# Kernel tuning notes

Measured on AMD Instinct MI355X. Metric: run time of the kernel, lower is better.

The kernel has to match this reference:

```python
import jax, jax.numpy as jnp
import numpy as np

B, S, D = 1, 4096, 2048
M = 4                  # compression rate
NC = S // M            # compressed slots
TOPK = 512
NH, C = 16, 64         # query heads, head dim
DC = 512               # query compression dim
NG, DG = 4, 512        # output projection groups, intermediate dim
CI, NHI = 64, 4        # indexer head dim, indexer heads
ROPE = 32              # partial rope dims (last ROPE of C)
EPS = 1e-6
NEG = -1e30


def _ln(x, w, b):
    mu = x.mean(-1, keepdims=True)
    var = ((x - mu) ** 2).mean(-1, keepdims=True)
    return (x - mu) * jax.lax.rsqrt(var + EPS) * w + b


def _rope(q, pos):
    # partial RoPE on the last ROPE dims of q [B,S,NH,C]; keys are NOT rotated (faithful)
    x_part, x_rope = q[..., :C - ROPE], q[..., C - ROPE:]
    x0, x1 = x_rope[..., 0::2], x_rope[..., 1::2]
    inv = 1.0 / (10000.0 ** (jnp.arange(0, ROPE, 2, dtype=jnp.float32) / ROPE))
    ang = pos[:, None].astype(jnp.float32) * inv[None]           # [S, ROPE/2]
    cos = jnp.cos(ang)[None, :, None, :]
    sin = jnp.sin(ang)[None, :, None, :]
    r = x0 * cos - x1 * sin
    i = x0 * sin + x1 * cos
    rot = jnp.stack([r, i], -1).reshape(x_rope.shape)
    return jnp.concatenate([x_part, rot], -1)


def reference(x, w_kv_a, w_kv_b, w_z_a, w_z_b, b_a, b_b, w_dq, w_iuq, w_w, w_k,
              w_uq, o_down, o_up, kvn_w, kvn_b, qn_w, qn_b, sink_logits):
    pos = jnp.arange(S)
    # ---- token-level compressor: windowed (2m-wide, m-stride) per-channel softmax ----
    c_a = (x @ w_kv_a).reshape(B, NC, M, C)
    c_b = (x @ w_kv_b).reshape(B, NC, M, C)
    z_a = (x @ w_z_a).reshape(B, NC, M, C)
    z_b = (x @ w_z_b).reshape(B, NC, M, C)
    prev_z = jnp.concatenate([jnp.full((B, 1, M, C), NEG, x.dtype), z_b[:, :-1]], 1)
    prev_c = jnp.concatenate([jnp.zeros((B, 1, M, C), x.dtype), c_b[:, :-1]], 1)
    logits = jnp.concatenate([prev_z + b_b, z_a + b_a], 2)        # [B,NC,2M,C]
    wts = jax.nn.softmax(logits, axis=2)
    compressed = (wts * jnp.concatenate([prev_c, c_a], 2)).sum(2)  # [B,NC,C]
    # ---- lightning indexer: relu multi-head scores + causal mask + top-k ----
    c_q = x @ w_dq                                                 # [B,S,DC]
    q_i = (c_q @ w_iuq).reshape(B, S, NHI, CI)
    hw = x @ w_w                                                   # [B,S,NHI]
    k_orig = x.reshape(B, NC, M, D).mean(2)
    k_proj = k_orig @ w_k                                          # [B,NC,CI]
    dot = jnp.einsum('bshc,bkc->bskh', q_i, k_proj)
    iscores = (jax.nn.relu(dot) * hw[:, :, None, :]).sum(-1)       # [B,S,NC]
    imask = jnp.arange(NC)[None, None, :] < pos[None, :, None]     # NC//S + 1 == 1
    iscores = jnp.where(imask, iscores, -jnp.inf)
    _, top_idx = jax.lax.top_k(iscores, TOPK)                      # [B,S,K]
    # ---- sparse attention over gathered compressed KV ----
    q = (c_q @ w_uq).reshape(B, S, NH, C)
    kc = _ln(compressed, kvn_w, kvn_b)
    q = _rope(_ln(q, qn_w, qn_b), pos)
    k_sel = kc[jnp.arange(B)[:, None, None], top_idx]              # [B,S,K,C]
    scores = jnp.einsum('bshc,bskc->bhsk', q, k_sel) / jnp.sqrt(jnp.float32(C))
    cmask = pos[None, None, :, None] < (top_idx[:, None, :, :] * M)
    scores = jnp.where(cmask, scores, -jnp.inf)
    e = jnp.exp(scores)
    denom = e.sum(-1, keepdims=True) + jnp.exp(sink_logits)[None, :, None, None]
    attn = e / denom                                               # sink-augmented softmax
    out = jnp.einsum('bhsk,bskc->bshc', attn, k_sel).reshape(B, S, NH * C)
    g = jnp.einsum('bsgd,gde->bsge', out.reshape(B, S, NG, (NH * C) // NG), o_down)
    return g.reshape(B, S, NG * DG) @ o_up


def setup_inputs() -> dict:
    key = jax.random.key(0)
    ks = jax.random.split(key, 20)
    lin = lambda k, fi, fo: jax.random.normal(k, (fi, fo), jnp.float32) / np.sqrt(fi)
    return {
        'x': jax.random.normal(ks[0], (B, S, D), jnp.float32),
        'w_kv_a': lin(ks[1], D, C), 'w_kv_b': lin(ks[2], D, C),
        'w_z_a': lin(ks[3], D, C), 'w_z_b': lin(ks[4], D, C),
        'b_a': 0.02 * jax.random.normal(ks[5], (M, C), jnp.float32),
        'b_b': 0.02 * jax.random.normal(ks[6], (M, C), jnp.float32),
        'w_dq': lin(ks[7], D, DC),
        'w_iuq': lin(ks[8], DC, CI * NHI),
        'w_w': lin(ks[9], D, NHI),
        'w_k': lin(ks[10], D, CI),
        'w_uq': lin(ks[11], DC, NH * C),
        'o_down': jax.random.normal(ks[12], (NG, (NH * C) // NG, DG), jnp.float32) / np.sqrt((NH * C) // NG),
        'o_up': lin(ks[13], NG * DG, D),
        'kvn_w': 1.0 + 0.02 * jax.random.normal(ks[14], (C,), jnp.float32),
        'kvn_b': 0.02 * jax.random.normal(ks[15], (C,), jnp.float32),
        'qn_w': 1.0 + 0.02 * jax.random.normal(ks[16], (C,), jnp.float32),
        'qn_b': 0.02 * jax.random.normal(ks[17], (C,), jnp.float32),
        'sink_logits': 0.02 * jax.random.normal(ks[18], (NH,), jnp.float32),
    }
```

## Files before the change

kernel.cpp:

```cpp
#include <hip/hip_runtime.h>
#include <math.h>

#define S_   4096
#define D_   2048
#define M_   4
#define NC_  1024
#define TOPK_ 512
#define NH_  16
#define C_   64
#define DC_  512
#define NG_  4
#define DG_  512
#define CI_  64
#define NHI_ 4
#define ROPE_ 32
#define EPS_ 1e-6f

typedef __attribute__((ext_vector_type(8))) short short8;
typedef __attribute__((ext_vector_type(4))) short short4v;
typedef __attribute__((ext_vector_type(4))) float floatx4;

__device__ inline unsigned short f2bf(float f) {
  unsigned u = __float_as_uint(f);
  u += 0x7fff + ((u >> 16) & 1);
  return (unsigned short)(u >> 16);
}
__device__ inline float bf2f(unsigned short h) {
  return __uint_as_float(((unsigned)h) << 16);
}

#define GLD16(src, dst) __builtin_amdgcn_global_load_lds( \
    (const __attribute__((address_space(1))) unsigned int*)(src), \
    (__attribute__((address_space(3))) unsigned int*)(dst), 16, 0, 0)

__global__ __launch_bounds__(256) void gemm_bf16_64(
    const unsigned short* __restrict__ A, const unsigned short* __restrict__ Bt,
    float* __restrict__ Cf, unsigned short* __restrict__ Cb,
    int K, int lda, int ldb, int ldc,
    long long Az, long long Bz, long long Cz) {
  int zz = blockIdx.z;
  A += (size_t)zz * Az;
  Bt += (size_t)zz * Bz;
  if (Cf) Cf += (size_t)zz * Cz;
  if (Cb) Cb += (size_t)zz * Cz;
  __shared__ unsigned short As[2 * 2 * 64 * 32];
  __shared__ unsigned short Bs[2 * 2 * 128 * 32];
  int tid = threadIdx.x;
  int bm = blockIdx.y * 64, bn = blockIdx.x * 128;
  int lane = tid & 63, wid = tid >> 6;
  int wm = (wid & 1) * 32, wn = (wid >> 1) * 64;
  int qd = lane >> 4, m16 = lane & 15;

  floatx4 acc[2][4];
#pragma unroll
  for (int i = 0; i < 2; ++i)
#pragma unroll
    for (int j = 0; j < 4; ++j) acc[i][j] = (floatx4){0.f, 0.f, 0.f, 0.f};

  auto stage = [&](int buf, int kt) {
#pragma unroll
    for (int h = 0; h < 2; ++h) {
      {
        int rr = tid >> 2, ss = tid & 3;
        int gg = ss ^ ((rr >> 1) & 3);
        GLD16(A + (size_t)(bm + rr) * lda + kt + h * 32 + gg * 8,
              &As[(buf * 2 + h) * 2048 + tid * 8]);
      }
#pragma unroll
      for (int i = 0; i < 2; ++i) {
        int idx = tid + 256 * i;
        int rr = idx >> 2, ss = idx & 3;
        int gg = ss ^ ((rr >> 1) & 3);
        GLD16(Bt + (size_t)(bn + rr) * ldb + kt + h * 32 + gg * 8,
              &Bs[(buf * 2 + h) * 4096 + idx * 8]);
      }
    }
  };
  auto compute = [&](int buf) {
#pragma unroll
    for (int h = 0; h < 2; ++h) {
      const unsigned short* Ab = &As[(buf * 2 + h) * 2048];
      const unsigned short* Bb = &Bs[(buf * 2 + h) * 4096];
      short8 af[2], bfr[4];
#pragma unroll
      for (int mi = 0; mi < 2; ++mi) {
        int r = wm + mi * 16 + m16;
        int slot = qd ^ ((r >> 1) & 3);
        af[mi] = *(const short8*)&Ab[r * 32 + slot * 8];
      }
#pragma unroll
      for (int ni = 0; ni < 4; ++ni) {
        int r = wn + ni * 16 + m16;
        int slot = qd ^ ((r >> 1) & 3);
        bfr[ni] = *(const short8*)&Bb[r * 32 + slot * 8];
      }
#pragma unroll
      for (int mi = 0; mi < 2; ++mi)
#pragma unroll
        for (int ni = 0; ni < 4; ++ni)
          acc[mi][ni] = __builtin_amdgcn_mfma_f32_16x16x32_bf16(af[mi], bfr[ni], acc[mi][ni], 0, 0, 0);
    }
  };

  stage(0, 0);
  __syncthreads();
  int cur = 0;
  for (int kt = 64; kt < K; kt += 64) {
    stage(cur ^ 1, kt);
    compute(cur);
    __syncthreads();
    cur ^= 1;
  }
  compute(cur);

#pragma unroll
  for (int mi = 0; mi < 2; ++mi)
#pragma unroll
    for (int ni = 0; ni < 4; ++ni) {
      int col = bn + wn + ni * 16 + m16;
#pragma unroll
      for (int rg = 0; rg < 4; ++rg) {
        int row = bm + wm + mi * 16 + qd * 4 + rg;
        if (Cb)
          Cb[(size_t)row * ldc + col] = f2bf(acc[mi][ni][rg]);
        else
          Cf[(size_t)row * ldc + col] = acc[mi][ni][rg];
      }
    }
}

__global__ __launch_bounds__(256) void gemm_bf16_128(
    const unsigned short* __restrict__ A, const unsigned short* __restrict__ Bt,
    float* __restrict__ Cf, unsigned short* __restrict__ Cb,
    int K, int lda, int ldb, int ldc,
    long long Az, long long Bz, long long Cz) {
  int zz = blockIdx.z;
  A += (size_t)zz * Az;
  Bt += (size_t)zz * Bz;
  if (Cf) Cf += (size_t)zz * Cz;
  if (Cb) Cb += (size_t)zz * Cz;
  __shared__ unsigned short As[2 * 2 * 128 * 32];
  __shared__ unsigned short Bs[2 * 2 * 128 * 32];
  int tid = threadIdx.x;
  int bm = blockIdx.y * 128, bn = blockIdx.x * 128;
  int lane = tid & 63, wid = tid >> 6;
  int wm = (wid & 1) * 64, wn = (wid >> 1) * 64;
  int qd = lane >> 4, m16 = lane & 15;

  floatx4 acc[4][4];
#pragma unroll
  for (int i = 0; i < 4; ++i)
#pragma unroll
    for (int j = 0; j < 4; ++j) acc[i][j] = (floatx4){0.f, 0.f, 0.f, 0.f};

  auto stage = [&](int buf, int kt) {
#pragma unroll
    for (int h = 0; h < 2; ++h) {
#pragma unroll
      for (int i = 0; i < 2; ++i) {
        int idx = tid + 256 * i;
        int rr = idx >> 2, ss = idx & 3;
        int gg = ss ^ ((rr >> 1) & 3);
        GLD16(A + (size_t)(bm + rr) * lda + kt + h * 32 + gg * 8,
              &As[(buf * 2 + h) * 4096 + idx * 8]);
        GLD16(Bt + (size_t)(bn + rr) * ldb + kt + h * 32 + gg * 8,
              &Bs[(buf * 2 + h) * 4096 + idx * 8]);
      }
    }
  };
  auto compute = [&](int buf) {
#pragma unroll
    for (int h = 0; h < 2; ++h) {
      const unsigned short* Ab = &As[(buf * 2 + h) * 4096];
      const unsigned short* Bb = &Bs[(buf * 2 + h) * 4096];
      short8 af[4], bfr[4];
#pragma unroll
      for (int mi = 0; mi < 4; ++mi) {
        int r = wm + mi * 16 + m16;
        int slot = qd ^ ((r >> 1) & 3);
        af[mi] = *(const short8*)&Ab[r * 32 + slot * 8];
      }
#pragma unroll
      for (int ni = 0; ni < 4; ++ni) {
        int r = wn + ni * 16 + m16;
        int slot = qd ^ ((r >> 1) & 3);
        bfr[ni] = *(const short8*)&Bb[r * 32 + slot * 8];
      }
#pragma unroll
      for (int mi = 0; mi < 4; ++mi)
#pragma unroll
        for (int ni = 0; ni < 4; ++ni)
          acc[mi][ni] = __builtin_amdgcn_mfma_f32_16x16x32_bf16(af[mi], bfr[ni], acc[mi][ni], 0, 0, 0);
    }
  };

  stage(0, 0);
  __syncthreads();
  int cur = 0;
  for (int kt = 64; kt < K; kt += 64) {
    stage(cur ^ 1, kt);
    compute(cur);
    __syncthreads();
    cur ^= 1;
  }
  compute(cur);

#pragma unroll
  for (int mi = 0; mi < 4; ++mi)
#pragma unroll
    for (int ni = 0; ni < 4; ++ni) {
      int col = bn + wn + ni * 16 + m16;
#pragma unroll
      for (int rg = 0; rg < 4; ++rg) {
        int row = bm + wm + mi * 16 + qd * 4 + rg;
        if (Cb)
          Cb[(size_t)row * ldc + col] = f2bf(acc[mi][ni][rg]);
        else
          Cf[(size_t)row * ldc + col] = acc[mi][ni][rg];
      }
    }
}

__global__ __launch_bounds__(256) void gemm_bf16_split_64(
    const unsigned short* __restrict__ Ah, const unsigned short* __restrict__ Al,
    const unsigned short* __restrict__ Bh, const unsigned short* __restrict__ Bl,
    float* __restrict__ Cf, int K, int lda, int ldb, int ldc,
    long long Az, long long Bz, long long Cz) {
  int zz = blockIdx.z;
  Ah += (size_t)zz * Az; Al += (size_t)zz * Az;
  Bh += (size_t)zz * Bz; Bl += (size_t)zz * Bz;
  Cf += (size_t)zz * Cz;
  __shared__ unsigned short Ash[64 * 32];
  __shared__ unsigned short Asl[64 * 32];
  __shared__ unsigned short Bsh[128 * 32];
  __shared__ unsigned short Bsl[128 * 32];
  int tid = threadIdx.x;
  int bm = blockIdx.y * 64, bn = blockIdx.x * 128;
  int lane = tid & 63, wid = tid >> 6;
  int wm = (wid & 1) * 32, wn = (wid >> 1) * 64;
  int qd = lane >> 4, m16 = lane & 15;

  floatx4 acc[2][4];
#pragma unroll
  for (int i = 0; i < 2; ++i)
#pragma unroll
    for (int j = 0; j < 4; ++j) acc[i][j] = (floatx4){0.f, 0.f, 0.f, 0.f};

  for (int k0 = 0; k0 < K; k0 += 32) {
    {
      int r = tid >> 2, sl = tid & 3;
      int g = sl ^ ((r >> 1) & 3);
      size_t aoff = (size_t)(bm + r) * lda + k0 + g * 8;
      GLD16(Ah + aoff, &Ash[tid * 8]);
      GLD16(Al + aoff, &Asl[tid * 8]);
    }
#pragma unroll
    for (int i = 0; i < 2; ++i) {
      int idx = tid + 256 * i;
      int r = idx >> 2, sl = idx & 3;
      int g = sl ^ ((r >> 1) & 3);
      size_t boff = (size_t)(bn + r) * ldb + k0 + g * 8;
      GLD16(Bh + boff, &Bsh[idx * 8]);
      GLD16(Bl + boff, &Bsl[idx * 8]);
    }
    __syncthreads();
    short8 afh[2], afl[2], bfh[4], bfl[4];
#pragma unroll
    for (int mi = 0; mi < 2; ++mi) {
      int r = wm + mi * 16 + m16;
      int slot = qd ^ ((r >> 1) & 3);
      afh[mi] = *(const short8*)&Ash[r * 32 + slot * 8];
      afl[mi] = *(const short8*)&Asl[r * 32 + slot * 8];
    }
#pragma unroll
    for (int ni = 0; ni < 4; ++ni) {
      int r = wn + ni * 16 + m16;
      int slot = qd ^ ((r >> 1) & 3);
      bfh[ni] = *(const short8*)&Bsh[r * 32 + slot * 8];
      bfl[ni] = *(const short8*)&Bsl[r * 32 + slot * 8];
    }
#pragma unroll
    for (int mi = 0; mi < 2; ++mi)
#pragma unroll
      for (int ni = 0; ni < 4; ++ni) {
        acc[mi][ni] = __builtin_amdgcn_mfma_f32_16x16x32_bf16(afh[mi], bfh[ni], acc[mi][ni], 0, 0, 0);
        acc[mi][ni] = __builtin_amdgcn_mfma_f32_16x16x32_bf16(afh[mi], bfl[ni], acc[mi][ni], 0, 0, 0);
        acc[mi][ni] = __builtin_amdgcn_mfma_f32_16x16x32_bf16(afl[mi], bfh[ni], acc[mi][ni], 0, 0, 0);
      }
    __syncthreads();
  }
#pragma unroll
  for (int mi = 0; mi < 2; ++mi)
#pragma unroll
    for (int ni = 0; ni < 4; ++ni) {
      int col = bn + wn + ni * 16 + m16;
#pragma unroll
      for (int rg = 0; rg < 4; ++rg) {
        int row = bm + wm + mi * 16 + qd * 4 + rg;
        Cf[(size_t)row * ldc + col] = acc[mi][ni][rg];
      }
    }
}

__global__ __launch_bounds__(256) void gemm_bf16_split_128(
    const unsigned short* __restrict__ Ah, const unsigned short* __restrict__ Al,
    const unsigned short* __restrict__ Bh, const unsigned short* __restrict__ Bl,
    float* __restrict__ Cf, int K, int lda, int ldb, int ldc,
    long long Az, long long Bz, long long Cz) {
  int zz = blockIdx.z;
  Ah += (size_t)zz * Az; Al += (size_t)zz * Az;
  Bh += (size_t)zz * Bz; Bl += (size_t)zz * Bz;
  Cf += (size_t)zz * Cz;
  __shared__ unsigned short Ash[2 * 128 * 32];
  __shared__ unsigned short Asl[2 * 128 * 32];
  __shared__ unsigned short Bsh[2 * 128 * 32];
  __shared__ unsigned short Bsl[2 * 128 * 32];
  int tid = threadIdx.x;
  int bm = blockIdx.y * 128, bn = blockIdx.x * 128;
  int lane = tid & 63, wid = tid >> 6;
  int wm = (wid & 1) * 64, wn = (wid >> 1) * 64;
  int qd = lane >> 4, m16 = lane & 15;

  floatx4 acc[4][4];
#pragma unroll
  for (int i = 0; i < 4; ++i)
#pragma unroll
    for (int j = 0; j < 4; ++j) acc[i][j] = (floatx4){0.f, 0.f, 0.f, 0.f};

  auto stage = [&](int buf, int kt) {
#pragma unroll
    for (int i = 0; i < 2; ++i) {
      int idx = tid + 256 * i;
      int rr = idx >> 2, ss = idx & 3;
      int gg = ss ^ ((rr >> 1) & 3);
      size_t aoff = (size_t)(bm + rr) * lda + kt + gg * 8;
      size_t boff = (size_t)(bn + rr) * ldb + kt + gg * 8;
      GLD16(Ah + aoff, &Ash[buf * 4096 + idx * 8]);
      GLD16(Al + aoff, &Asl[buf * 4096 + idx * 8]);
      GLD16(Bh + boff, &Bsh[buf * 4096 + idx * 8]);
      GLD16(Bl + boff, &Bsl[buf * 4096 + idx * 8]);
    }
  };
  auto compute = [&](int buf) {
    const unsigned short* Ahb = &Ash[buf * 4096];
    const unsigned short* Alb = &Asl[buf * 4096];
    const unsigned short* Bhb = &Bsh[buf * 4096];
    const unsigned short* Blb = &Bsl[buf * 4096];
    short8 afh[4], afl[4], bfh[4], bfl[4];
#pragma unroll
    for (int mi = 0; mi < 4; ++mi) {
      int r = wm + mi * 16 + m16;
      int slot = qd ^ ((r >> 1) & 3);
      afh[mi] = *(const short8*)&Ahb[r * 32 + slot * 8];
      afl[mi] = *(const short8*)&Alb[r * 32 + slot * 8];
    }
#pragma unroll
    for (int ni = 0; ni < 4; ++ni) {
      int r = wn + ni * 16 + m16;
      int slot = qd ^ ((r >> 1) & 3);
      bfh[ni] = *(const short8*)&Bhb[r * 32 + slot * 8];
      bfl[ni] = *(const short8*)&Blb[r * 32 + slot * 8];
    }
#pragma unroll
    for (int mi = 0; mi < 4; ++mi)
#pragma unroll
      for (int ni = 0; ni < 4; ++ni) {
        acc[mi][ni] = __builtin_amdgcn_mfma_f32_16x16x32_bf16(afh[mi], bfh[ni], acc[mi][ni], 0, 0, 0);
        acc[mi][ni] = __builtin_amdgcn_mfma_f32_16x16x32_bf16(afh[mi], bfl[ni], acc[mi][ni], 0, 0, 0);
        acc[mi][ni] = __builtin_amdgcn_mfma_f32_16x16x32_bf16(afl[mi], bfh[ni], acc[mi][ni], 0, 0, 0);
      }
  };

  stage(0, 0);
  __syncthreads();
  int cur = 0;
  for (int kt = 32; kt < K; kt += 32) {
    stage(cur ^ 1, kt);
    compute(cur);
    __syncthreads();
    cur ^= 1;
  }
  compute(cur);

#pragma unroll
  for (int mi = 0; mi < 4; ++mi)
#pragma unroll
    for (int ni = 0; ni < 4; ++ni) {
      int col = bn + wn + ni * 16 + m16;
#pragma unroll
      for (int rg = 0; rg < 4; ++rg) {
        int row = bm + wm + mi * 16 + qd * 4 + rg;
        Cf[(size_t)row * ldc + col] = acc[mi][ni][rg];
      }
    }
}

__global__ void reduce_f32(const float* __restrict__ P, float* __restrict__ C, int n, int z) {
  int i = (blockIdx.x * 256 + threadIdx.x) * 4;
  if (i >= n) return;
  float4 a = *(const float4*)&P[i];
  for (int s = 1; s < z; ++s) {
    float4 b = *(const float4*)&P[(size_t)s * n + i];
    a.x += b.x; a.y += b.y; a.z += b.z; a.w += b.w;
  }
  *(float4*)&C[i] = a;
}

__global__ void reduce_cast_split(const float* __restrict__ P, unsigned short* __restrict__ hi,
                                  unsigned short* __restrict__ lo, int n, int z) {
  int i = (blockIdx.x * 256 + threadIdx.x) * 4;
  if (i >= n) return;
  float4 a = *(const float4*)&P[i];
  for (int s = 1; s < z; ++s) {
    float4 b = *(const float4*)&P[(size_t)s * n + i];
    a.x += b.x; a.y += b.y; a.z += b.z; a.w += b.w;
  }
  ushort4 h = make_ushort4(f2bf(a.x), f2bf(a.y), f2bf(a.z), f2bf(a.w));
  ushort4 l = make_ushort4(f2bf(a.x - bf2f(h.x)), f2bf(a.y - bf2f(h.y)),
                           f2bf(a.z - bf2f(h.z)), f2bf(a.w - bf2f(h.w)));
  *(ushort4*)&hi[i] = h;
  *(ushort4*)&lo[i] = l;
}

__global__ __launch_bounds__(256) void iscores_mfma(
    const unsigned short* __restrict__ Ah, const unsigned short* __restrict__ Al,
    const unsigned short* __restrict__ Bh, const unsigned short* __restrict__ Bl,
    const float* __restrict__ hw, float* __restrict__ isc) {
  int bm = blockIdx.y * 128, bn = blockIdx.x * 128;
  if (bn > (bm >> 2) + 30) return;
  __shared__ unsigned short Ash[128 * 32];
  __shared__ unsigned short Asl[128 * 32];
  __shared__ unsigned short Bsh[128 * 32];
  __shared__ unsigned short Bsl[128 * 32];
  int tid = threadIdx.x;
  int lane = tid & 63, wid = tid >> 6;
  int wm = (wid >> 1) * 64, wn = (wid & 1) * 64;
  int qd = lane >> 4, m16 = lane & 15;

  floatx4 acc[4][4];
#pragma unroll
  for (int i = 0; i < 4; ++i)
#pragma unroll
    for (int j = 0; j < 4; ++j) acc[i][j] = (floatx4){0.f, 0.f, 0.f, 0.f};

#pragma unroll
  for (int k0 = 0; k0 < 64; k0 += 32) {
#pragma unroll
    for (int i = 0; i < 2; ++i) {
      int idx = tid + 256 * i;
      int r = idx >> 2, s = idx & 3;
      int g = s ^ ((r >> 1) & 3);
      size_t aoff = (size_t)(bm + r) * 64 + k0 + g * 8;
      size_t boff = (size_t)(bn + r) * 64 + k0 + g * 8;
      GLD16(Ah + aoff, &Ash[idx * 8]);
      GLD16(Al + aoff, &Asl[idx * 8]);
      GLD16(Bh + boff, &Bsh[idx * 8]);
      GLD16(Bl + boff, &Bsl[idx * 8]);
    }
    __syncthreads();
    short8 afh[4], afl[4], bfh[4], bfl[4];
#pragma unroll
    for (int mi = 0; mi < 4; ++mi) {
      int r = wm + mi * 16 + m16;
      int slot = qd ^ ((r >> 1) & 3);
      afh[mi] = *(const short8*)&Ash[r * 32 + slot * 8];
      afl[mi] = *(const short8*)&Asl[r * 32 + slot * 8];
    }
#pragma unroll
    for (int ni = 0; ni < 4; ++ni) {
      int r = wn + ni * 16 + m16;
      int slot = qd ^ ((r >> 1) & 3);
      bfh[ni] = *(const short8*)&Bsh[r * 32 + slot * 8];
      bfl[ni] = *(const short8*)&Bsl[r * 32 + slot * 8];
    }
#pragma unroll
    for (int mi = 0; mi < 4; ++mi)
#pragma unroll
      for (int ni = 0; ni < 4; ++ni) {
        acc[mi][ni] = __builtin_amdgcn_mfma_f32_16x16x32_bf16(afh[mi], bfh[ni], acc[mi][ni], 0, 0, 0);
        acc[mi][ni] = __builtin_amdgcn_mfma_f32_16x16x32_bf16(afh[mi], bfl[ni], acc[mi][ni], 0, 0, 0);
        acc[mi][ni] = __builtin_amdgcn_mfma_f32_16x16x32_bf16(afl[mi], bfh[ni], acc[mi][ni], 0, 0, 0);
      }
    __syncthreads();
  }
#pragma unroll
  for (int mi = 0; mi < 4; ++mi) {
    int tok = ((bm + wm + mi * 16) >> 2) + qd;
    float4 hwv = *(const float4*)&hw[tok * 4];
#pragma unroll
    for (int ni = 0; ni < 4; ++ni) {
      floatx4 a = acc[mi][ni];
      float v = fmaxf(a[0], 0.f) * hwv.x + fmaxf(a[1], 0.f) * hwv.y +
                fmaxf(a[2], 0.f) * hwv.z + fmaxf(a[3], 0.f) * hwv.w;
      int col = bn + wn + ni * 16 + m16;
      isc[(size_t)tok * NC_ + col] = (col < tok) ? v : -__builtin_inff();
    }
  }
}

#define BM 64
#define BN 64
#define BK 16
#define KSL_ 16
#define KSLICE_ 128
__global__ __launch_bounds__(256) void gemm_f32_splitk(
    const float* __restrict__ A, const float* __restrict__ B,
    float* __restrict__ P, int lda, int ldb) {
  __shared__ float As[BK][BM + 4];
  __shared__ float Bs[BK][BN + 4];
  int tid = threadIdx.x;
  int bm = blockIdx.y * BM;
  int kbase = blockIdx.x * KSLICE_;
  int tr = tid >> 4;
  int tc = tid & 15;
  float acc[4][4] = {{0.f}};
  for (int k0 = kbase; k0 < kbase + KSLICE_; k0 += BK) {
    int ac = tid & 15;
    int ar0 = tid >> 4;
#pragma unroll
    for (int i = 0; i < 4; ++i) {
      int r = ar0 + 16 * i;
      As[ac][r] = A[(size_t)(bm + r) * lda + k0 + ac];
    }
    int bc = tid & 63;
    int br0 = tid >> 6;
#pragma unroll
    for (int i = 0; i < 4; ++i) {
      int r = br0 + 4 * i;
      Bs[r][bc] = B[(size_t)(k0 + r) * ldb + bc];
    }
    __syncthreads();
#pragma unroll
    for (int kk = 0; kk < BK; ++kk) {
      float4 av = *(const float4*)&As[kk][tr * 4];
      float4 bv = *(const float4*)&Bs[kk][tc * 4];
      float a[4] = {av.x, av.y, av.z, av.w};
      float b[4] = {bv.x, bv.y, bv.z, bv.w};
#pragma unroll
      for (int i = 0; i < 4; ++i)
#pragma unroll
        for (int j = 0; j < 4; ++j) acc[i][j] += a[i] * b[j];
    }
    __syncthreads();
  }
  float* Pb = P + (size_t)blockIdx.x * (NC_ * CI_);
#pragma unroll
  for (int i = 0; i < 4; ++i) {
    float4 v = make_float4(acc[i][0], acc[i][1], acc[i][2], acc[i][3]);
    *(float4*)&Pb[(size_t)(bm + tr * 4 + i) * CI_ + tc * 4] = v;
  }
}

__global__ void reduce_splitk(const float* __restrict__ P, float* __restrict__ C) {
  int i = blockIdx.x * 256 + threadIdx.x;
  if (i >= NC_ * CI_) return;
  float a = 0.f;
#pragma unroll
  for (int s = 0; s < KSL_; ++s) a += P[(size_t)s * (NC_ * CI_) + i];
  C[i] = a;
}

__global__ void cast_bf16(const float* __restrict__ in, unsigned short* __restrict__ out, int n) {
  int i = (blockIdx.x * 256 + threadIdx.x) * 4;
  if (i >= n) return;
  float4 v = *(const float4*)&in[i];
  ushort4 o = make_ushort4(f2bf(v.x), f2bf(v.y), f2bf(v.z), f2bf(v.w));
  *(ushort4*)&out[i] = o;
}

__global__ void cast_split(const float* __restrict__ in, unsigned short* __restrict__ hi,
                           unsigned short* __restrict__ lo, int n) {
  int i = (blockIdx.x * 256 + threadIdx.x) * 4;
  if (i >= n) return;
  float4 v = *(const float4*)&in[i];
  ushort4 h = make_ushort4(f2bf(v.x), f2bf(v.y), f2bf(v.z), f2bf(v.w));
  ushort4 l = make_ushort4(f2bf(v.x - bf2f(h.x)), f2bf(v.y - bf2f(h.y)),
                           f2bf(v.z - bf2f(h.z)), f2bf(v.w - bf2f(h.w)));
  *(ushort4*)&hi[i] = h;
  *(ushort4*)&lo[i] = l;
}

__device__ inline float wave_sum64(float v) {
#pragma unroll
  for (int off = 32; off > 0; off >>= 1) v += __shfl_xor(v, off, 64);
  return v;
}

__global__ __launch_bounds__(512) void cast_split_hw(
    const float* __restrict__ x, unsigned short* __restrict__ hi,
    unsigned short* __restrict__ lo, const float* __restrict__ ww,
    float* __restrict__ hw) {
  int s = blockIdx.x, tid = threadIdx.x;
  size_t i = (size_t)s * D_ + tid * 4;
  float4 v = *(const float4*)&x[i];
  ushort4 h = make_ushort4(f2bf(v.x), f2bf(v.y), f2bf(v.z), f2bf(v.w));
  ushort4 l = make_ushort4(f2bf(v.x - bf2f(h.x)), f2bf(v.y - bf2f(h.y)),
                           f2bf(v.z - bf2f(h.z)), f2bf(v.w - bf2f(h.w)));
  *(ushort4*)&hi[i] = h;
  *(ushort4*)&lo[i] = l;
  const float* wr = ww + tid * 16;
  float a0 = v.x * wr[0] + v.y * wr[4] + v.z * wr[8]  + v.w * wr[12];
  float a1 = v.x * wr[1] + v.y * wr[5] + v.z * wr[9]  + v.w * wr[13];
  float a2 = v.x * wr[2] + v.y * wr[6] + v.z * wr[10] + v.w * wr[14];
  float a3 = v.x * wr[3] + v.y * wr[7] + v.z * wr[11] + v.w * wr[15];
  a0 = wave_sum64(a0); a1 = wave_sum64(a1);
  a2 = wave_sum64(a2); a3 = wave_sum64(a3);
  __shared__ float red[8][4];
  int wid = tid >> 6, lane = tid & 63;
  if (lane == 0) { red[wid][0] = a0; red[wid][1] = a1; red[wid][2] = a2; red[wid][3] = a3; }
  __syncthreads();
  if (tid < 4) {
    float acc = 0.f;
#pragma unroll
    for (int w2 = 0; w2 < 8; ++w2) acc += red[w2][tid];
    hw[s * 4 + tid] = acc;
  }
}

__global__ __launch_bounds__(256) void transpose_cast(
    const float* __restrict__ in, unsigned short* __restrict__ out, int K, int N,
    long long inz, long long outz) {
  in += (size_t)blockIdx.z * inz;
  out += (size_t)blockIdx.z * outz;
  __shared__ float t[32][33];
  int k0 = blockIdx.x * 32, n0 = blockIdx.y * 32;
  int tx = threadIdx.x & 31, ty = threadIdx.x >> 5;
#pragma unroll
  for (int i = 0; i < 4; ++i)
    t[ty * 4 + i][tx] = in[(size_t)(k0 + ty * 4 + i) * N + n0 + tx];
  __syncthreads();
#pragma unroll
  for (int i = 0; i < 4; ++i)
    out[(size_t)(n0 + ty * 4 + i) * K + k0 + tx] = f2bf(t[tx][ty * 4 + i]);
}

__global__ __launch_bounds__(256) void transpose_cast_split(
    const float* __restrict__ in, unsigned short* __restrict__ outh,
    unsigned short* __restrict__ outl, int K, int N) {
  __shared__ float t[32][33];
  int k0 = blockIdx.x * 32, n0 = blockIdx.y * 32;
  int tx = threadIdx.x & 31, ty = threadIdx.x >> 5;
#pragma unroll
  for (int i = 0; i < 4; ++i)
    t[ty * 4 + i][tx] = in[(size_t)(k0 + ty * 4 + i) * N + n0 + tx];
  __syncthreads();
#pragma unroll
  for (int i = 0; i < 4; ++i) {
    float v = t[tx][ty * 4 + i];
    unsigned short h = f2bf(v);
    outh[(size_t)(n0 + ty * 4 + i) * K + k0 + tx] = h;
    outl[(size_t)(n0 + ty * 4 + i) * K + k0 + tx] = f2bf(v - bf2f(h));
  }
}

__global__ void mean4_kernel(const float* __restrict__ x, float* __restrict__ ko) {
  int i = blockIdx.x * 256 + threadIdx.x;
  if (i >= NC_ * D_) return;
  int j = i >> 11, d = i & (D_ - 1);
  const float* p = x + (size_t)j * 4 * D_ + d;
  ko[i] = 0.25f * (p[0] + p[D_] + p[2 * D_] + p[3 * D_]);
}

__global__ void gate_kernel(const float* __restrict__ c4,
                            const float* __restrict__ ba, const float* __restrict__ bb,
                            float* __restrict__ comp) {
  int i = blockIdx.x * 256 + threadIdx.x;
  if (i >= NC_ * C_) return;
  int j = i >> 6, c = i & 63;
  float lg[8], vv[8];
#pragma unroll
  for (int m = 0; m < 4; ++m) {
    if (j == 0) {
      lg[m] = -1e30f + bb[m * C_ + c];
      vv[m] = 0.f;
    } else {
      int row = (j - 1) * 4 + m;
      lg[m] = c4[(size_t)row * 256 + 192 + c] + bb[m * C_ + c];
      vv[m] = c4[(size_t)row * 256 + 64 + c];
    }
    int row2 = j * 4 + m;
    lg[4 + m] = c4[(size_t)row2 * 256 + 128 + c] + ba[m * C_ + c];
    vv[4 + m] = c4[(size_t)row2 * 256 + 0 + c];
  }
  float mx = lg[0];
#pragma unroll
  for (int t = 1; t < 8; ++t) mx = fmaxf(mx, lg[t]);
  float se = 0.f, acc = 0.f;
#pragma unroll
  for (int t = 0; t < 8; ++t) {
    float e = expf(lg[t] - mx);
    se += e;
    acc += e * vv[t];
  }
  comp[i] = acc / se;
}

__global__ void ln_kc_kernel(const float* __restrict__ in, const float* __restrict__ w,
                             const float* __restrict__ b, unsigned short* __restrict__ kcb,
                             unsigned short* __restrict__ kcbT) {
  int row = blockIdx.x * 4 + (threadIdx.x >> 6);
  int c = threadIdx.x & 63;
  float v = in[(size_t)row * C_ + c];
  float mu = wave_sum64(v) * (1.f / 64.f);
  float d = v - mu;
  float var = wave_sum64(d * d) * (1.f / 64.f);
  float y = d * (1.f / sqrtf(var + EPS_)) * w[c] + b[c];
  unsigned short h = f2bf(y);
  kcb[(size_t)row * C_ + c] = h;
  kcbT[(size_t)c * NC_ + row] = h;
}

__global__ void ln_rope_q_kernel(const float* __restrict__ quq, const float* __restrict__ w,
                                 const float* __restrict__ b, unsigned short* __restrict__ qb) {
  int row = blockIdx.x * 4 + (threadIdx.x >> 6);
  int s = row >> 4;
  int c = threadIdx.x & 63;
  float v = quq[(size_t)row * C_ + c];
  float mu = wave_sum64(v) * (1.f / 64.f);
  float d = v - mu;
  float var = wave_sum64(d * d) * (1.f / 64.f);
  float y = d * (1.f / sqrtf(var + EPS_)) * w[c] + b[c];
  float outv;
  float partner = __shfl_xor(y, 1, 64);
  if (c < C_ - ROPE_) {
    outv = y;
  } else {
    int p = (c - (C_ - ROPE_)) >> 1;
    float inv = powf(10000.f, -(2.f * (float)p) / (float)ROPE_);
    float ang = (float)s * inv;
    float cs = cosf(ang), sn = sinf(ang);
    if ((c & 1) == 0)
      outv = y * cs - partner * sn;
    else
      outv = partner * sn + y * cs;
  }
  qb[(size_t)row * C_ + c] = f2bf(outv * 0.125f);
}

#define MINF_ 0x007FFFFFu
__global__ __launch_bounds__(256) void topk_select_kernel(
    const float* __restrict__ isc, unsigned* __restrict__ sel) {
  __shared__ unsigned mv[NC_];
  __shared__ unsigned bins[256];
  __shared__ unsigned scan[256];
  __shared__ unsigned sB, sR;
  __shared__ unsigned selw[32];
  int s = blockIdx.x;
  int tid = threadIdx.x;
  for (int i = tid; i < NC_; i += 256) {
    if (i < s) {
      unsigned u = __float_as_uint(isc[(size_t)s * NC_ + i]);
      mv[i] = (u & 0x80000000u) ? ~u : (u | 0x80000000u);
    } else {
      mv[i] = MINF_;
    }
  }
  __syncthreads();
  unsigned K_rem = TOPK_;
  unsigned prefix = 0u;
  for (int lvl = 0; lvl < 4; ++lvl) {
    int shift = 24 - 8 * lvl;
    unsigned pm = (lvl == 0) ? 0u : (0xFFFFFFFFu << (32 - 8 * lvl));
    bins[tid] = 0u;
    __syncthreads();
    for (int i = tid; i < NC_; i += 256) {
      unsigned m = mv[i];
      if ((m & pm) == prefix) atomicAdd(&bins[(m >> shift) & 0xFFu], 1u);
    }
    __syncthreads();
    unsigned v = bins[tid];
    scan[tid] = v;
    __syncthreads();
    for (int off = 1; off < 256; off <<= 1) {
      unsigned add = (tid + off < 256) ? scan[tid + off] : 0u;
      __syncthreads();
      scan[tid] += add;
      __syncthreads();
    }
    unsigned gt = scan[tid] - v;
    if (gt < K_rem && K_rem <= gt + v) { sB = (unsigned)tid; sR = K_rem - gt; }
    __syncthreads();
    prefix |= (sB << shift);
    K_rem = sR;
    __syncthreads();
  }
  unsigned vstar = prefix;
  unsigned eq = 0;
#pragma unroll
  for (int j = 0; j < 4; ++j) eq += (mv[4 * tid + j] == vstar);
  scan[tid] = eq;
  __syncthreads();
  for (int off = 1; off < 256; off <<= 1) {
    unsigned add = (tid >= off) ? scan[tid - off] : 0u;
    __syncthreads();
    scan[tid] += add;
    __syncthreads();
  }
  unsigned rank0 = scan[tid] - eq;
  if (tid < 32) selw[tid] = 0u;
  __syncthreads();
  unsigned local = 0, bits = 0;
#pragma unroll
  for (int j = 0; j < 4; ++j) {
    unsigned m = mv[4 * tid + j];
    bool sb = (m > vstar) || (m == vstar && (rank0 + local) < K_rem);
    local += (m == vstar);
    if (sb) bits |= (1u << ((4 * tid + j) & 31));
  }
  if (bits) atomicOr(&selw[tid >> 3], bits);
  __syncthreads();
  if (tid < 32) sel[(size_t)s * 32 + tid] = selw[tid];
}

#define TS_ 8
__global__ __launch_bounds__(256) void attn_mfma_kernel(
    const unsigned short* __restrict__ qb, const unsigned short* __restrict__ kcb,
    const unsigned short* __restrict__ kcbT, const unsigned* __restrict__ sel,
    const float* __restrict__ sink, unsigned short* __restrict__ out) {
  __shared__ unsigned short kc_s[64 * 72];
  __shared__ unsigned short kct_s[64 * 72];
  __shared__ unsigned short p_s[128 * 72];
  __shared__ unsigned selw[TS_][32];
  __shared__ float dls[4][2][16];
  int tid = threadIdx.x;
  int s0 = blockIdx.x * TS_;
  int lane = tid & 63, w = tid >> 6;
  int qd = lane >> 4, m16 = lane & 15;

  for (int i = tid; i < TS_ * 32; i += 256)
    selw[i >> 5][i & 31] = sel[(size_t)(s0 + (i >> 5)) * 32 + (i & 31)];

  short8 qf[2][2];
#pragma unroll
  for (int tk = 0; tk < 2; ++tk)
#pragma unroll
    for (int ks = 0; ks < 2; ++ks)
      qf[tk][ks] = *(const short8*)&qb[(size_t)(s0 + 2 * w + tk) * 1024 + m16 * 64 + ks * 32 + qd * 8];

  floatx4 of[2][4];
#pragma unroll
  for (int i = 0; i < 2; ++i)
#pragma unroll
    for (int j = 0; j < 4; ++j) of[i][j] = (floatx4){0.f, 0.f, 0.f, 0.f};
  float dsum[2] = {0.f, 0.f};

  int ub = max(511, s0 + TS_ - 2);
  int ct_start = max(0, (s0 + 4) >> 8);
  int ct_end = min(16, (ub >> 6) + 1);

  for (int ct = ct_start; ct < ct_end; ++ct) {
    int c0 = ct * 64;
    __syncthreads();
    {
      int r = tid >> 2, cc = (tid & 3) * 16;
      *(short8*)&kc_s[r * 72 + cc]      = *(const short8*)&kcb[(size_t)(c0 + r) * 64 + cc];
      *(short8*)&kc_s[r * 72 + cc + 8]  = *(const short8*)&kcb[(size_t)(c0 + r) * 64 + cc + 8];
      *(short8*)&kct_s[r * 72 + cc]     = *(const short8*)&kcbT[(size_t)r * NC_ + c0 + cc];
      *(short8*)&kct_s[r * 72 + cc + 8] = *(const short8*)&kcbT[(size_t)r * NC_ + c0 + cc + 8];
    }
    __syncthreads();
#pragma unroll
    for (int mc = 0; mc < 4; ++mc) {
      short8 a0 = *(const short8*)&kc_s[(mc * 16 + m16) * 72 + qd * 8];
      short8 a1 = *(const short8*)&kc_s[(mc * 16 + m16) * 72 + 32 + qd * 8];
#pragma unroll
      for (int nt = 0; nt < 2; ++nt) {
        floatx4 sc = (floatx4){0.f, 0.f, 0.f, 0.f};
        sc = __builtin_amdgcn_mfma_f32_16x16x32_bf16(a0, qf[nt][0], sc, 0, 0, 0);
        sc = __builtin_amdgcn_mfma_f32_16x16x32_bf16(a1, qf[nt][1], sc, 0, 0, 0);
        int tokL = 2 * w + nt;
        int sG = s0 + tokL;
        short4v pv;
#pragma unroll
        for (int rg = 0; rg < 4; ++rg) {
          int cG = c0 + mc * 16 + qd * 4 + rg;
          bool ok = (((selw[tokL][cG >> 5] >> (cG & 31)) & 1u) != 0u) && (sG < cG * 4);
          float e = ok ? __expf(sc[rg]) : 0.f;
          dsum[nt] += e;
          pv[rg] = (short)f2bf(e);
        }
        *(short4v*)&p_s[(tokL * 16 + m16) * 72 + mc * 16 + qd * 4] = pv;
      }
    }
#pragma unroll
    for (int ks = 0; ks < 2; ++ks) {
      short8 pa0 = *(const short8*)&p_s[((2 * w + 0) * 16 + m16) * 72 + ks * 32 + qd * 8];
      short8 pa1 = *(const short8*)&p_s[((2 * w + 1) * 16 + m16) * 72 + ks * 32 + qd * 8];
#pragma unroll
      for (int nt = 0; nt < 4; ++nt) {
        short8 bv = *(const short8*)&kct_s[(nt * 16 + m16) * 72 + ks * 32 + qd * 8];
        of[0][nt] = __builtin_amdgcn_mfma_f32_16x16x32_bf16(pa0, bv, of[0][nt], 0, 0, 0);
        of[1][nt] = __builtin_amdgcn_mfma_f32_16x16x32_bf16(pa1, bv, of[1][nt], 0, 0, 0);
      }
    }
  }
#pragma unroll
  for (int nt = 0; nt < 2; ++nt) {
    dsum[nt] += __shfl_xor(dsum[nt], 16, 64);
    dsum[nt] += __shfl_xor(dsum[nt], 32, 64);
  }
  if (lane < 16) {
    float sk = __expf(sink[lane]);
    dls[w][0][lane] = dsum[0] + sk;
    dls[w][1][lane] = dsum[1] + sk;
  }
  __syncthreads();
#pragma unroll
  for (int tk = 0; tk < 2; ++tk)
#pragma unroll
    for (int nt = 0; nt < 4; ++nt) {
      floatx4 o = of[tk][nt];
#pragma unroll
      for (int rg = 0; rg < 4; ++rg) {
        int head = qd * 4 + rg;
        float dn = dls[w][tk][head];
        out[(size_t)(s0 + 2 * w + tk) * 1024 + head * 64 + nt * 16 + m16] = f2bf(o[rg] / dn);
      }
    }
}

#define OFF_QUQ    0u
#define OFF_Q      4194304u
#define OFF_XH     8388608u
#define OFF_XL     12582912u
#define OFF_PART   16777216u
#define OFF_KO     18874368u
#define OFF_C4     20971520u
#define OFF_CQF    22020096u
#define OFF_WTB    24117248u
#define OFF_CQH    25165824u
#define OFF_CQL    26214400u
#define OFF_WPACKT 27262976u
#define OFF_WDQTH  27525120u
#define OFF_WDQTL  28049408u
#define OFF_WIUQTH 28573696u
#define OFF_WIUQTL 28639232u
#define OFF_WUQT   28704768u
#define OFF_ODB    28966912u
#define OFF_OUPT   29229056u
#define OFF_HW     31326208u
#define OFF_COMP   31342592u
#define OFF_KC     31408128u
#define OFF_KPR    31473664u

extern "C" void kernel_launch(void* const* d_in, const int* in_sizes, int n_in,
                              void* d_out, int out_size, void* d_ws, size_t ws_size,
                              hipStream_t stream) {
  const float* x      = (const float*)d_in[0];
  const float* w_kv_a = (const float*)d_in[1];
  const float* w_kv_b = (const float*)d_in[2];
  const float* w_z_a  = (const float*)d_in[3];
  const float* w_z_b  = (const float*)d_in[4];
  const float* b_a    = (const float*)d_in[5];
  const float* b_b    = (const float*)d_in[6];
  const float* w_dq   = (const float*)d_in[7];
  const float* w_iuq  = (const float*)d_in[8];
  const float* w_w    = (const float*)d_in[9];
  const float* w_k    = (const float*)d_in[10];
  const float* w_uq   = (const float*)d_in[11];
  const float* o_down = (const float*)d_in[12];
  const float* o_up   = (const float*)d_in[13];
  const float* kvn_w  = (const float*)d_in[14];
  const float* kvn_b  = (const float*)d_in[15];
  const float* qn_w   = (const float*)d_in[16];
  const float* qn_b   = (const float*)d_in[17];
  const float* sink   = (const float*)d_in[18];
  float* out = (float*)d_out;
  float* ws = (float*)d_ws;

  float* quq   = ws + OFF_QUQ;
  float* isc   = ws + OFF_QUQ;
  unsigned short* qb = (unsigned short*)(ws + OFF_Q);
  unsigned short* xh = (unsigned short*)(ws + OFF_XH);
  unsigned short* xl = (unsigned short*)(ws + OFF_XL);
  unsigned* sel = (unsigned*)(ws + OFF_XL);
  float* part  = ws + OFF_PART;
  float* k_or  = ws + OFF_KO;
  unsigned short* attnb = (unsigned short*)(ws + OFF_KO);
  float* c4    = ws + OFF_C4;
  unsigned short* qih = (unsigned short*)(ws + OFF_CQF);
  unsigned short* qil = qih + S_ * NHI_ * CI_;
  unsigned short* kph = qil + S_ * NHI_ * CI_;
  unsigned short* kpl = kph + NC_ * CI_;
  unsigned short* wtb = (unsigned short*)(ws + OFF_WTB);
  unsigned short* cqh = (unsigned short*)(ws + OFF_CQH);
  unsigned short* cql = (unsigned short*)(ws + OFF_CQL);
  unsigned short* wpackT = (unsigned short*)(ws + OFF_WPACKT);
  unsigned short* wdqTh  = (unsigned short*)(ws + OFF_WDQTH);
  unsigned short* wdqTl  = (unsigned short*)(ws + OFF_WDQTL);
  unsigned short* wiuqTh = (unsigned short*)(ws + OFF_WIUQTH);
  unsigned short* wiuqTl = (unsigned short*)(ws + OFF_WIUQTL);
  unsigned short* wuqT   = (unsigned short*)(ws + OFF_WUQT);
  unsigned short* odb    = (unsigned short*)(ws + OFF_ODB);
  unsigned short* oupT   = (unsigned short*)(ws + OFF_OUPT);
  float* hw    = ws + OFF_HW;
  float* comp  = ws + OFF_COMP;
  unsigned short* kcb  = (unsigned short*)(ws + OFF_KC);
  unsigned short* kcbT = kcb + NC_ * C_;
  float* k_pr  = ws + OFF_KPR;

  dim3 blk(256);

  cast_split_hw<<<S_, dim3(512), 0, stream>>>(x, xh, xl, w_w, hw);
  transpose_cast<<<dim3(64, 2), blk, 0, stream>>>(w_kv_a, wpackT + 0 * 64 * 2048, D_, C_, 0, 0);
  transpose_cast<<<dim3(64, 2), blk, 0, stream>>>(w_kv_b, wpackT + 1 * 64 * 2048, D_, C_, 0, 0);
  transpose_cast<<<dim3(64, 2), blk, 0, stream>>>(w_z_a,  wpackT + 2 * 64 * 2048, D_, C_, 0, 0);
  transpose_cast<<<dim3(64, 2), blk, 0, stream>>>(w_z_b,  wpackT + 3 * 64 * 2048, D_, C_, 0, 0);
  transpose_cast_split<<<dim3(64, 16), blk, 0, stream>>>(w_dq, wdqTh, wdqTl, D_, DC_);
  transpose_cast_split<<<dim3(16, 8), blk, 0, stream>>>(w_iuq, wiuqTh, wiuqTl, DC_, NHI_ * CI_);
  transpose_cast<<<dim3(16, 32), blk, 0, stream>>>(w_uq, wuqT, DC_, NH_ * C_, 0, 0);
  cast_bf16<<<512, blk, 0, stream>>>(o_down, odb, NG_ * 256 * DG_);
  transpose_cast<<<dim3(64, 64), blk, 0, stream>>>(o_up, oupT, NG_ * DG_, D_, 0, 0);

  gemm_bf16_64<<<dim3(2, 32, 4), blk, 0, stream>>>(
      oupT, odb, nullptr, wtb, DG_, D_, DG_, NG_ * 256,
      (long long)DG_, (long long)256 * DG_, 256LL);

  mean4_kernel<<<8192, blk, 0, stream>>>(x, k_or);
  gemm_f32_splitk<<<dim3(KSL_, 16), blk, 0, stream>>>(k_or, w_k, part, D_, CI_);
  reduce_splitk<<<256, blk, 0, stream>>>(part, k_pr);

  gemm_bf16_split_128<<<dim3(4, 32, 4), blk, 0, stream>>>(xh, xl, wdqTh, wdqTl, ws,
                                                          512, D_, D_, DC_, 512, 512, (long long)S_ * DC_);
  reduce_cast_split<<<2048, blk, 0, stream>>>(ws, cqh, cql, S_ * DC_, 4);
  gemm_bf16_64<<<dim3(2, 64, 4), blk, 0, stream>>>(xh, wpackT, part, nullptr,
                                                   512, D_, D_, 256, 512, 512, (long long)S_ * 256);
  reduce_f32<<<1024, blk, 0, stream>>>(part, c4, S_ * 256, 4);
  gemm_bf16_split_64<<<dim3(2, 64, 4), blk, 0, stream>>>(cqh, cql, wiuqTh, wiuqTl, part,
                                                         128, DC_, DC_, 256, 128, 128, (long long)S_ * 256);
  reduce_cast_split<<<1024, blk, 0, stream>>>(part, qih, qil, S_ * 256, 4);
  gemm_bf16_64<<<dim3(8, 64, 1), blk, 0, stream>>>(cqh, wuqT, quq, nullptr,
                                                   DC_, DC_, DC_, NH_ * C_, 0, 0, 0);

  gate_kernel<<<256, blk, 0, stream>>>(c4, b_a, b_b, comp);
  ln_kc_kernel<<<256, blk, 0, stream>>>(comp, kvn_w, kvn_b, kcb, kcbT);

  ln_rope_q_kernel<<<16384, blk, 0, stream>>>(quq, qn_w, qn_b, qb);

  cast_split<<<64, blk, 0, stream>>>(k_pr, kph, kpl, NC_ * CI_);
  iscores_mfma<<<dim3(8, 128), blk, 0, stream>>>(qih, qil, kph, kpl, hw, isc);
  topk_select_kernel<<<S_, blk, 0, stream>>>(isc, sel);

  attn_mfma_kernel<<<S_ / TS_, blk, 0, stream>>>(qb, kcb, kcbT, sel, sink, attnb);

  gemm_bf16_128<<<dim3(16, 32, 1), blk, 0, stream>>>(attnb, wtb, out, nullptr,
                                                     NG_ * 256, NH_ * C_, NG_ * 256, D_, 0, 0, 0);
}
```

Baseline: 433.8 us.

## Fuse mean4 into cast kernel, XCD-swizzle GEMM blocks, wave-scan in top-k

The 4-row mean of x is folded into the cast/split/hw kernel, so x is read once and one launch disappears. All three bf16 GEMM kernels now remap block indices so neighbouring tiles land on the same XCD, aiming for better L2 reuse. The top-k radix select swaps its LDS Hillis-Steele scans, which needed many barriers, for wave shuffle scans plus a small cross-wave offset step. The cast kernel now keeps four rows per block, which raises register use and cuts the block count by a factor of four.

```diff
diff --git a/kernel.cpp b/kernel.cpp
--- a/kernel.cpp
+++ b/kernel.cpp
@@ -33,12 +33,24 @@
     (const __attribute__((address_space(1))) unsigned int*)(src), \
     (__attribute__((address_space(3))) unsigned int*)(dst), 16, 0, 0)
 
+__device__ inline void xcd_remap(int& bx, int& by, int& bz) {
+  int nx = gridDim.x, ny = gridDim.y;
+  int flat = blockIdx.x + nx * (blockIdx.y + ny * blockIdx.z);
+  int nwg = nx * ny * (int)gridDim.z;
+  int swz = (flat & 7) * (nwg >> 3) + (flat >> 3);
+  bx = swz % nx;
+  int t = swz / nx;
+  by = t % ny;
+  bz = t / ny;
+}
+
 __global__ __launch_bounds__(256) void gemm_bf16_64(
     const unsigned short* __restrict__ A, const unsigned short* __restrict__ Bt,
     float* __restrict__ Cf, unsigned short* __restrict__ Cb,
     int K, int lda, int ldb, int ldc,
     long long Az, long long Bz, long long Cz) {
-  int zz = blockIdx.z;
+  int bx, by, zz;
+  xcd_remap(bx, by, zz);
   A += (size_t)zz * Az;
   Bt += (size_t)zz * Bz;
   if (Cf) Cf += (size_t)zz * Cz;
@@ -46,7 +58,7 @@
   __shared__ unsigned short As[2 * 2 * 64 * 32];
   __shared__ unsigned short Bs[2 * 2 * 128 * 32];
   int tid = threadIdx.x;
-  int bm = blockIdx.y * 64, bn = blockIdx.x * 128;
+  int bm = by * 64, bn = bx * 128;
   int lane = tid & 63, wid = tid >> 6;
   int wm = (wid & 1) * 32, wn = (wid >> 1) * 64;
   int qd = lane >> 4, m16 = lane & 15;
@@ -226,7 +238,8 @@
     const unsigned short* __restrict__ Bh, const unsigned short* __restrict__ Bl,
     float* __restrict__ Cf, int K, int lda, int ldb, int ldc,
     long long Az, long long Bz, long long Cz) {
-  int zz = blockIdx.z;
+  int bx, by, zz;
+  xcd_remap(bx, by, zz);
   Ah += (size_t)zz * Az; Al += (size_t)zz * Az;
   Bh += (size_t)zz * Bz; Bl += (size_t)zz * Bz;
   Cf += (size_t)zz * Cz;
@@ -235,7 +248,7 @@
   __shared__ unsigned short Bsh[128 * 32];
   __shared__ unsigned short Bsl[128 * 32];
   int tid = threadIdx.x;
-  int bm = blockIdx.y * 64, bn = blockIdx.x * 128;
+  int bm = by * 64, bn = bx * 128;
   int lane = tid & 63, wid = tid >> 6;
   int wm = (wid & 1) * 32, wn = (wid >> 1) * 64;
   int qd = lane >> 4, m16 = lane & 15;
@@ -307,7 +320,8 @@
     const unsigned short* __restrict__ Bh, const unsigned short* __restrict__ Bl,
     float* __restrict__ Cf, int K, int lda, int ldb, int ldc,
     long long Az, long long Bz, long long Cz) {
-  int zz = blockIdx.z;
+  int bx, by, zz;
+  xcd_remap(bx, by, zz);
   Ah += (size_t)zz * Az; Al += (size_t)zz * Az;
   Bh += (size_t)zz * Bz; Bl += (size_t)zz * Bz;
   Cf += (size_t)zz * Cz;
@@ -316,7 +330,7 @@
   __shared__ unsigned short Bsh[2 * 128 * 32];
   __shared__ unsigned short Bsl[2 * 128 * 32];
   int tid = threadIdx.x;
-  int bm = blockIdx.y * 128, bn = blockIdx.x * 128;
+  int bm = by * 128, bn = bx * 128;
   int lane = tid & 63, wid = tid >> 6;
   int wm = (wid & 1) * 64, wn = (wid >> 1) * 64;
   int qd = lane >> 4, m16 = lane & 15;
@@ -586,34 +600,53 @@
   return v;
 }
 
-__global__ __launch_bounds__(512) void cast_split_hw(
+__global__ __launch_bounds__(512) void cast_split_hw_mean(
     const float* __restrict__ x, unsigned short* __restrict__ hi,
     unsigned short* __restrict__ lo, const float* __restrict__ ww,
-    float* __restrict__ hw) {
-  int s = blockIdx.x, tid = threadIdx.x;
-  size_t i = (size_t)s * D_ + tid * 4;
-  float4 v = *(const float4*)&x[i];
-  ushort4 h = make_ushort4(f2bf(v.x), f2bf(v.y), f2bf(v.z), f2bf(v.w));
-  ushort4 l = make_ushort4(f2bf(v.x - bf2f(h.x)), f2bf(v.y - bf2f(h.y)),
-                           f2bf(v.z - bf2f(h.z)), f2bf(v.w - bf2f(h.w)));
-  *(ushort4*)&hi[i] = h;
-  *(ushort4*)&lo[i] = l;
-  const float* wr = ww + tid * 16;
-  float a0 = v.x * wr[0] + v.y * wr[4] + v.z * wr[8]  + v.w * wr[12];
-  float a1 = v.x * wr[1] + v.y * wr[5] + v.z * wr[9]  + v.w * wr[13];
-  float a2 = v.x * wr[2] + v.y * wr[6] + v.z * wr[10] + v.w * wr[14];
-  float a3 = v.x * wr[3] + v.y * wr[7] + v.z * wr[11] + v.w * wr[15];
-  a0 = wave_sum64(a0); a1 = wave_sum64(a1);
-  a2 = wave_sum64(a2); a3 = wave_sum64(a3);
-  __shared__ float red[8][4];
+    float* __restrict__ hw, float* __restrict__ ko) {
+  int j = blockIdx.x, tid = threadIdx.x;
+  int d0 = tid * 4;
+  const float* wr = ww + d0 * 4;
+  float4 v[4];
+  float a[4][4];
+#pragma unroll
+  for (int m = 0; m < 4; ++m) {
+    size_t i = (size_t)(j * 4 + m) * D_ + d0;
+    v[m] = *(const float4*)&x[i];
+    ushort4 h = make_ushort4(f2bf(v[m].x), f2bf(v[m].y), f2bf(v[m].z), f2bf(v[m].w));
+    ushort4 l = make_ushort4(f2bf(v[m].x - bf2f(h.x)), f2bf(v[m].y - bf2f(h.y)),
+                             f2bf(v[m].z - bf2f(h.z)), f2bf(v[m].w - bf2f(h.w)));
+    *(ushort4*)&hi[i] = h;
+    *(ushort4*)&lo[i] = l;
+    a[m][0] = v[m].x * wr[0] + v[m].y * wr[4] + v[m].z * wr[8]  + v[m].w * wr[12];
+    a[m][1] = v[m].x * wr[1] + v[m].y * wr[5] + v[m].z * wr[9]  + v[m].w * wr[13];
+    a[m][2] = v[m].x * wr[2] + v[m].y * wr[6] + v[m].z * wr[10] + v[m].w * wr[14];
+    a[m][3] = v[m].x * wr[3] + v[m].y * wr[7] + v[m].z * wr[11] + v[m].w * wr[15];
+  }
+  float4 s4;
+  s4.x = 0.25f * (v[0].x + v[1].x + v[2].x + v[3].x);
+  s4.y = 0.25f * (v[0].y + v[1].y + v[2].y + v[3].y);
+  s4.z = 0.25f * (v[0].z + v[1].z + v[2].z + v[3].z);
+  s4.w = 0.25f * (v[0].w + v[1].w + v[2].w + v[3].w);
+  *(float4*)&ko[(size_t)j * D_ + d0] = s4;
+#pragma unroll
+  for (int m = 0; m < 4; ++m)
+#pragma unroll
+    for (int h2 = 0; h2 < 4; ++h2) a[m][h2] = wave_sum64(a[m][h2]);
+  __shared__ float red[8][16];
   int wid = tid >> 6, lane = tid & 63;
-  if (lane == 0) { red[wid][0] = a0; red[wid][1] = a1; red[wid][2] = a2; red[wid][3] = a3; }
+  if (lane == 0) {
+#pragma unroll
+    for (int m = 0; m < 4; ++m)
+#pragma unroll
+      for (int h2 = 0; h2 < 4; ++h2) red[wid][m * 4 + h2] = a[m][h2];
+  }
   __syncthreads();
-  if (tid < 4) {
+  if (tid < 16) {
     float acc = 0.f;
 #pragma unroll
     for (int w2 = 0; w2 < 8; ++w2) acc += red[w2][tid];
-    hw[s * 4 + tid] = acc;
+    hw[(size_t)(j * 4 + (tid >> 2)) * 4 + (tid & 3)] = acc;
   }
 }
 
@@ -651,14 +684,6 @@
     outh[(size_t)(n0 + ty * 4 + i) * K + k0 + tx] = h;
     outl[(size_t)(n0 + ty * 4 + i) * K + k0 + tx] = f2bf(v - bf2f(h));
   }
-}
-
-__global__ void mean4_kernel(const float* __restrict__ x, float* __restrict__ ko) {
-  int i = blockIdx.x * 256 + threadIdx.x;
-  if (i >= NC_ * D_) return;
-  int j = i >> 11, d = i & (D_ - 1);
-  const float* p = x + (size_t)j * 4 * D_ + d;
-  ko[i] = 0.25f * (p[0] + p[D_] + p[2 * D_] + p[3 * D_]);
 }
 
 __global__ void gate_kernel(const float* __restrict__ c4,
@@ -742,11 +767,13 @@
     const float* __restrict__ isc, unsigned* __restrict__ sel) {
   __shared__ unsigned mv[NC_];
   __shared__ unsigned bins[256];
-  __shared__ unsigned scan[256];
+  __shared__ unsigned wsum[4];
   __shared__ unsigned sB, sR;
   __shared__ unsigned selw[32];
   int s = blockIdx.x;
   int tid = threadIdx.x;
+  int w = tid >> 6, lane = tid & 63;
+  if (tid < 32) selw[tid] = 0u;
   for (int i = tid; i < NC_; i += 256) {
     if (i < s) {
       unsigned u = __float_as_uint(isc[(size_t)s * NC_ + i]);
@@ -769,36 +796,45 @@
     }
     __syncthreads();
     unsigned v = bins[tid];
-    scan[tid] = v;
-    __syncthreads();
-    for (int off = 1; off < 256; off <<= 1) {
-      unsigned add = (tid + off < 256) ? scan[tid + off] : 0u;
-      __syncthreads();
-      scan[tid] += add;
-      __syncthreads();
-    }
-    unsigned gt = scan[tid] - v;
+    unsigned p = v;
+#pragma unroll
+    for (int off = 1; off < 64; off <<= 1) {
+      unsigned n = __shfl_up(p, (unsigned)off, 64);
+      if (lane >= off) p += n;
+    }
+    if (lane == 63) wsum[w] = p;
+    __syncthreads();
+    unsigned T = 0, woff = 0;
+#pragma unroll
+    for (int i = 0; i < 4; ++i) {
+      unsigned x_ = wsum[i];
+      T += x_;
+      if (i < w) woff += x_;
+    }
+    p += woff;
+    unsigned gt = T - p;
     if (gt < K_rem && K_rem <= gt + v) { sB = (unsigned)tid; sR = K_rem - gt; }
     __syncthreads();
     prefix |= (sB << shift);
     K_rem = sR;
-    __syncthreads();
   }
   unsigned vstar = prefix;
   unsigned eq = 0;
 #pragma unroll
   for (int j = 0; j < 4; ++j) eq += (mv[4 * tid + j] == vstar);
-  scan[tid] = eq;
+  unsigned rp = eq;
+#pragma unroll
+  for (int off = 1; off < 64; off <<= 1) {
+    unsigned n = __shfl_up(rp, (unsigned)off, 64);
+    if (lane >= off) rp += n;
+  }
+  if (lane == 63) wsum[w] = rp;
   __syncthreads();
-  for (int off = 1; off < 256; off <<= 1) {
-    unsigned add = (tid >= off) ? scan[tid - off] : 0u;
-    __syncthreads();
-    scan[tid] += add;
-    __syncthreads();
-  }
-  unsigned rank0 = scan[tid] - eq;
-  if (tid < 32) selw[tid] = 0u;
-  __syncthreads();
+  unsigned woff2 = 0;
+#pragma unroll
+  for (int i = 0; i < 4; ++i)
+    if (i < w) woff2 += wsum[i];
+  unsigned rank0 = rp + woff2 - eq;
   unsigned local = 0, bits = 0;
 #pragma unroll
   for (int j = 0; j < 4; ++j) {
@@ -1001,7 +1037,7 @@
 
   dim3 blk(256);
 
-  cast_split_hw<<<S_, dim3(512), 0, stream>>>(x, xh, xl, w_w, hw);
+  cast_split_hw_mean<<<NC_, dim3(512), 0, stream>>>(x, xh, xl, w_w, hw, k_or);
   transpose_cast<<<dim3(64, 2), blk, 0, stream>>>(w_kv_a, wpackT + 0 * 64 * 2048, D_, C_, 0, 0);
   transpose_cast<<<dim3(64, 2), blk, 0, stream>>>(w_kv_b, wpackT + 1 * 64 * 2048, D_, C_, 0, 0);
   transpose_cast<<<dim3(64, 2), blk, 0, stream>>>(w_z_a,  wpackT + 2 * 64 * 2048, D_, C_, 0, 0);
@@ -1016,7 +1052,6 @@
       oupT, odb, nullptr, wtb, DG_, D_, DG_, NG_ * 256,
       (long long)DG_, (long long)256 * DG_, 256LL);
 
-  mean4_kernel<<<8192, blk, 0, stream>>>(x, k_or);
   gemm_f32_splitk<<<dim3(KSL_, 16), blk, 0, stream>>>(k_or, w_k, part, D_, CI_);
   reduce_splitk<<<256, blk, 0, stream>>>(part, k_pr);
 
```

Result: faster. 411.2 us (-5.2%).
